# Optimization experiments

Hardware: AMD Instinct MI355X
Metric: run time of the kernel (lower is better)

## Reference

```python
import jax, jax.numpy as jnp
import numpy as np

T, B, I, H = 512, 64, 512, 512


def setup_inputs() -> dict:
    key = jax.random.key(0)
    ks = jax.random.split(key, 24)
    s = (1.0 / H) ** 0.5  # uniform_(-sqrt(1/hidden), sqrt(1/hidden))
    u = lambda k, shape: jax.random.uniform(k, shape, jnp.float32, -s, s)
    inp = {
        "x": jax.random.normal(ks[0], (T, B, I), jnp.float32),
        "h0": u(ks[1], (B, H)),
        "c0": u(ks[2], (B, H)),
    }
    j = 3
    for g in ("ii", "if", "ig", "io"):
        inp["W_" + g] = u(ks[j], (I, H)); j += 1
        inp["b_" + g] = u(ks[j], (H,)); j += 1
    for g in ("hi", "hf", "hg", "ho"):
        inp["W_" + g] = u(ks[j], (H, H)); j += 1
        inp["b_" + g] = u(ks[j], (H,)); j += 1
    return inp


def reference(x, h0, c0, W_ii, b_ii, W_if, b_if, W_ig, b_ig, W_io, b_io,
              W_hi, b_hi, W_hf, b_hf, W_hg, b_hg, W_ho, b_ho):
    # Concatenating per-gate weights is mathematically identical to the 8
    # separate matmuls + bias adds in the source cell.
    Wx = jnp.concatenate([W_ii, W_if, W_ig, W_io], axis=1)        # [I, 4H]
    Wh = jnp.concatenate([W_hi, W_hf, W_hg, W_ho], axis=1)        # [H, 4H]
    b = jnp.concatenate([b_ii + b_hi, b_if + b_hf, b_ig + b_hg, b_io + b_ho])
    # Precompute all input projections in one big GEMM: [T, B, 4H]
    xg = jnp.einsum('tbi,ih->tbh', x, Wx) + b

    def step(carry, xg_t):
        h, c = carry
        gates = xg_t + h @ Wh                                      # [B, 4H]
        i_g, f_g, g_g, o_g = jnp.split(gates, 4, axis=-1)
        i = jax.nn.sigmoid(i_g)
        f = jax.nn.sigmoid(f_g)
        g = jnp.tanh(g_g)
        o = jax.nn.sigmoid(o_g)
        c1 = f * c + i * g
        h1 = o * c1  # NOTE: source applies o * c_1 WITHOUT tanh(c_1)
        return (h1, c1), h1

    (hT, cT), out = jax.lax.scan(step, (h0, c0), xg)               # out: [T, B, H]
    return (out, hT, cT)
```

## Files before the change

kernel.cpp:

```cpp
#include <hip/hip_runtime.h>
#include <stdint.h>


typedef __attribute__((ext_vector_type(8))) short    short8;
typedef __attribute__((ext_vector_type(4))) float    f32x4;
typedef __attribute__((ext_vector_type(4))) unsigned u32x4;
typedef __attribute__((ext_vector_type(2))) unsigned u32x2;

#define XG_OFF    0ull
#define WBT_OFF   134217728ull
#define BIAS_OFF  136314880ull
#define HW_OFF    136323072ull

static __device__ __forceinline__ unsigned short f2bf(float f) {
  unsigned u = __float_as_uint(f);
  unsigned r = (u + 0x7FFFu + ((u >> 16) & 1u)) >> 16;
  return (unsigned short)r;
}
static __device__ __forceinline__ float bf2f(unsigned short u) {
  return __uint_as_float(((unsigned)u) << 16);
}
static __device__ __forceinline__ float sigmoidf_(float x) {
  return 1.0f / (1.0f + __expf(-x));
}
static __device__ __forceinline__ float tanhf_(float x) {
  return 1.0f - 2.0f / (__expf(2.0f * x) + 1.0f);
}

__global__ void lstm_prep(const float* __restrict__ W_ii, const float* __restrict__ W_if,
                          const float* __restrict__ W_ig, const float* __restrict__ W_io,
                          const float* __restrict__ b_ii, const float* __restrict__ b_if,
                          const float* __restrict__ b_ig, const float* __restrict__ b_io,
                          const float* __restrict__ b_hi, const float* __restrict__ b_hf,
                          const float* __restrict__ b_hg, const float* __restrict__ b_ho,
                          const float* __restrict__ h0, unsigned char* ws)
{
  unsigned short*     WbT  = (unsigned short*)(ws + WBT_OFF);
  float*              bias = (float*)(ws + BIAS_OFF);
  unsigned long long* hw64 = (unsigned long long*)(ws + HW_OFF);

  const int gid = blockIdx.x * blockDim.x + threadIdx.x;
  const int gsz = gridDim.x * blockDim.x;

  for (int i = gid; i < 4 * 512 * 512; i += gsz) {
    int g = i >> 18, rem = i & 262143, c = rem >> 9, k = rem & 511;
    const float* W = (g == 0) ? W_ii : (g == 1) ? W_if : (g == 2) ? W_ig : W_io;
    WbT[(size_t)(g * 512 + c) * 512 + k] = f2bf(W[(size_t)k * 512 + c]);
  }
  for (int i = gid; i < 2048; i += gsz) {
    int g = i >> 9, c = i & 511;
    const float* bi = (g == 0) ? b_ii : (g == 1) ? b_if : (g == 2) ? b_ig : b_io;
    const float* bh = (g == 0) ? b_hi : (g == 1) ? b_hf : (g == 2) ? b_hg : b_ho;
    bias[i] = bi[c] + bh[c];
  }
  for (int i = gid; i < 64 * 256; i += gsz) {
    int r = i >> 8, wc = i & 255;
    int gb = r >> 4, row = r & 15, wsl = wc >> 6, c = wc & 63;
    unsigned lo = f2bf(h0[(size_t)r * 512 + wc * 2]);
    unsigned hi = f2bf(h0[(size_t)r * 512 + wc * 2 + 1]);
    hw64[((size_t)(gb * 4 + wsl) * 16 + row) * 64 + c] =
        (unsigned long long)(lo | (hi << 16));
  }
  for (int i = gid; i < 64 * 256; i += gsz)
    hw64[16384 + i] = 0xFFFFFFFF00000000ull;
}

__global__ __launch_bounds__(256) void xproj_gemm(const float* __restrict__ x,
                                                  unsigned char* ws)
{
  const unsigned short* WbT  = (const unsigned short*)(ws + WBT_OFF);
  const float*          bias = (const float*)(ws + BIAS_OFF);
  unsigned short*       xg   = (unsigned short*)(ws + XG_OFF);

  __shared__ unsigned short As[128 * 64];
  __shared__ unsigned short Bs[128 * 64];

  const int bid  = (int)blockIdx.x;
  const int bidx = (bid & 7) * 512 + (bid >> 3);
  const int bm = bidx >> 4, bn = bidx & 15;
  const int row0 = bm * 128, col0 = bn * 128;

  const int tid = threadIdx.x, lane = tid & 63, w = tid >> 6;
  const int wr = w >> 1, wc = w & 1;

  f32x4 acc[4][4] = {};

  for (int k0 = 0; k0 < 512; k0 += 64) {
    __syncthreads();
#pragma unroll
    for (int u = 0; u < 8; ++u) {
      int idx = u * 256 + tid;
      int r = idx >> 4, quad = idx & 15;
      const float4 v = *reinterpret_cast<const float4*>(
          &x[(size_t)(row0 + r) * 512 + k0 + quad * 4]);
      uint2 p;
      p.x = (unsigned)f2bf(v.x) | ((unsigned)f2bf(v.y) << 16);
      p.y = (unsigned)f2bf(v.z) | ((unsigned)f2bf(v.w) << 16);
      *reinterpret_cast<uint2*>(&As[r * 64 + quad * 4]) = p;
    }
#pragma unroll
    for (int u = 0; u < 4; ++u) {
      int idx = u * 256 + tid;
      int cl = idx >> 3, ch = idx & 7;
      *reinterpret_cast<uint4*>(&Bs[cl * 64 + ch * 8]) =
          *reinterpret_cast<const uint4*>(&WbT[(size_t)(col0 + cl) * 512 + k0 + ch * 8]);
    }
    __syncthreads();
#pragma unroll
    for (int kk = 0; kk < 64; kk += 32) {
      short8 a[4], b[4];
#pragma unroll
      for (int m = 0; m < 4; ++m)
        a[m] = *reinterpret_cast<const short8*>(
            &As[(wr * 64 + m * 16 + (lane & 15)) * 64 + kk + (lane >> 4) * 8]);
#pragma unroll
      for (int n = 0; n < 4; ++n)
        b[n] = *reinterpret_cast<const short8*>(
            &Bs[(wc * 64 + n * 16 + (lane & 15)) * 64 + kk + (lane >> 4) * 8]);
#pragma unroll
      for (int m = 0; m < 4; ++m)
#pragma unroll
        for (int n = 0; n < 4; ++n)
          acc[m][n] = __builtin_amdgcn_mfma_f32_16x16x32_bf16(a[m], b[n], acc[m][n], 0, 0, 0);
    }
  }
#pragma unroll
  for (int m = 0; m < 4; ++m) {
    int rowtile = bm * 8 + wr * 4 + m;
#pragma unroll
    for (int n = 0; n < 4; ++n) {
      int coltile = bn * 8 + wc * 4 + n;
      float bv = bias[coltile * 16 + (lane & 15)];
      uint2 p;
      p.x = (unsigned)f2bf(acc[m][n][0] + bv) | ((unsigned)f2bf(acc[m][n][1] + bv) << 16);
      p.y = (unsigned)f2bf(acc[m][n][2] + bv) | ((unsigned)f2bf(acc[m][n][3] + bv) << 16);
      *reinterpret_cast<uint2*>(&xg[((size_t)rowtile * 128 + coltile) * 256 + lane * 4]) = p;
    }
  }
}

__global__ __launch_bounds__(256, 1) void lstm_rec(
    const float* __restrict__ Whi, const float* __restrict__ Whf,
    const float* __restrict__ Whg, const float* __restrict__ Who,
    const float* __restrict__ c0, unsigned char* ws, float* __restrict__ out)
{
  const int gb = (int)blockIdx.x & 3;
  const int gc = (int)blockIdx.x >> 2;
  const int tid = threadIdx.x, lane = tid & 63, w = tid >> 6;

  const unsigned short* xg = (const unsigned short*)(ws + XG_OFF);
  unsigned long long*   hw64 = (unsigned long long*)(ws + HW_OFF);

  __shared__ unsigned hdat[4][1024];
  __shared__ float glds[2][4][4][16][16];

  short8 bhi[4][4], blo[4][4];
  {
    const int colg = gc * 16 + (lane & 15);
    const int krow = (lane >> 4) * 8;
#pragma unroll
    for (int g = 0; g < 4; ++g) {
      const float* P = (g == 0) ? Whi : (g == 1) ? Whf : (g == 2) ? Whg : Who;
#pragma unroll
      for (int kkl = 0; kkl < 4; ++kkl) {
        short8 h8, l8;
#pragma unroll
        for (int i = 0; i < 8; ++i) {
          int k = w * 128 + kkl * 32 + krow + i;
          float wv = P[(size_t)k * 512 + colg];
          unsigned short hb = f2bf(wv);
          h8[i] = (short)hb;
          l8[i] = (short)f2bf(wv - bf2f(hb));
        }
        bhi[g][kkl] = h8; blo[g][kkl] = l8;
      }
    }
  }

  const int crow = tid >> 4, ccol = tid & 15;
  float c = c0[(size_t)(gb * 16 + crow) * 512 + gc * 16 + ccol];

  float* hT = out + 16777216;
  float* cT = out + 16777216 + 32768;
  const int e_ix = (crow >> 2) * 64 + ccol * 4 + (crow & 3);
  int bleft = 30000000;

  for (int t = 0; t < 512; ++t) {
    const size_t xb = (size_t)(t * 4 + gb) * 128 * 256;
    float xgi = bf2f(xg[xb + (size_t)(0 * 32 + gc) * 256 + e_ix]);
    float xgf = bf2f(xg[xb + (size_t)(1 * 32 + gc) * 256 + e_ix]);
    float xgg = bf2f(xg[xb + (size_t)(2 * 32 + gc) * 256 + e_ix]);
    float xgo = bf2f(xg[xb + (size_t)(3 * 32 + gc) * 256 + e_ix]);

    const int par = t & 1;
    const unsigned long long* blk =
        hw64 + (size_t)((par * 4 + gb) * 4 + w) * 1024;
    const unsigned tagw = (unsigned)t;

    u32x4 dv[8];
    const char* lbase = (const char*)blk + lane * 16;
    for (;;) {
#pragma unroll
      for (int i = 0; i < 8; ++i)
        asm volatile("global_load_dwordx4 %0, %1, off sc0 sc1"
                     : "=v"(dv[i]) : "v"(lbase + (size_t)i * 1024));
      asm volatile("s_waitcnt vmcnt(0)"
                   : "+v"(dv[0]), "+v"(dv[1]), "+v"(dv[2]), "+v"(dv[3]),
                     "+v"(dv[4]), "+v"(dv[5]), "+v"(dv[6]), "+v"(dv[7])
                   :: "memory");
      bool ok = true;
#pragma unroll
      for (int i = 0; i < 8; ++i)
        ok = ok && (dv[i][1] == tagw) && (dv[i][3] == tagw);
      if (__all(ok) || --bleft <= 0) break;
      __builtin_amdgcn_s_sleep(1);
    }

#pragma unroll
    for (int i = 0; i < 8; ++i) {
      int k = i * 128 + lane * 2;
      int row = k >> 6;
      int sw = k ^ ((row & 7) << 2);
      u32x2 p2; p2[0] = dv[i][0]; p2[1] = dv[i][2];
      *reinterpret_cast<u32x2*>(&hdat[w][sw]) = p2;
    }
    asm volatile("s_waitcnt lgkmcnt(0)" ::: "memory");
    __builtin_amdgcn_sched_barrier(0);

    f32x4 acc[4] = {};
#pragma unroll
    for (int kkl = 0; kkl < 4; ++kkl) {
      int base = (lane & 15) * 64 + kkl * 16 + (lane >> 4) * 4;
      int sw = base ^ ((lane & 7) << 2);
      union { u32x4 v; short8 s; } fr;
      fr.v = *reinterpret_cast<const u32x4*>(&hdat[w][sw]);
#pragma unroll
      for (int g = 0; g < 4; ++g) {
        acc[g] = __builtin_amdgcn_mfma_f32_16x16x32_bf16(fr.s, bhi[g][kkl], acc[g], 0, 0, 0);
        acc[g] = __builtin_amdgcn_mfma_f32_16x16x32_bf16(fr.s, blo[g][kkl], acc[g], 0, 0, 0);
      }
    }
#pragma unroll
    for (int g = 0; g < 4; ++g)
#pragma unroll
      for (int j = 0; j < 4; ++j)
        glds[par][w][g][(lane >> 4) * 4 + j][lane & 15] = acc[g][j];
    __syncthreads();

    float gi = xgi, gf = xgf, gg = xgg, go = xgo;
#pragma unroll
    for (int ww = 0; ww < 4; ++ww) {
      gi += glds[par][ww][0][crow][ccol];
      gf += glds[par][ww][1][crow][ccol];
      gg += glds[par][ww][2][crow][ccol];
      go += glds[par][ww][3][crow][ccol];
    }
    float iv = sigmoidf_(gi), fv = sigmoidf_(gf), gv = tanhf_(gg), ov = sigmoidf_(go);
    c = fv * c + iv * gv;
    float h = ov * c;

    if (t != 511) {
      float hp = __shfl_xor(h, 1);
      if ((ccol & 1) == 0) {
        unsigned data = (unsigned)f2bf(h) | ((unsigned)f2bf(hp) << 16);
        u32x2 wp; wp[0] = data; wp[1] = (unsigned)(t + 1);
        unsigned long long* dst =
            hw64 + ((size_t)((((t + 1) & 1) * 4 + gb) * 4 + (gc >> 3)) * 16 + crow) * 64 +
            (gc & 7) * 8 + (ccol >> 1);
        asm volatile("global_store_dwordx2 %0, %1, off sc0 sc1"
                     :: "v"(dst), "v"(wp) : "memory");
      }
    }

    out[(size_t)t * 32768 + (size_t)(gb * 16 + crow) * 512 + gc * 16 + ccol] = h;
    if (t == 511) {
      hT[(size_t)(gb * 16 + crow) * 512 + gc * 16 + ccol] = h;
      cT[(size_t)(gb * 16 + crow) * 512 + gc * 16 + ccol] = c;
    }
  }
}

extern "C" void kernel_launch(void* const* d_in, const int* in_sizes, int n_in,
                              void* d_out, int out_size, void* d_ws, size_t ws_size,
                              hipStream_t stream)
{
  const float* x    = (const float*)d_in[0];
  const float* h0   = (const float*)d_in[1];
  const float* c0   = (const float*)d_in[2];
  const float* W_ii = (const float*)d_in[3];
  const float* b_ii = (const float*)d_in[4];
  const float* W_if = (const float*)d_in[5];
  const float* b_if = (const float*)d_in[6];
  const float* W_ig = (const float*)d_in[7];
  const float* b_ig = (const float*)d_in[8];
  const float* W_io = (const float*)d_in[9];
  const float* b_io = (const float*)d_in[10];
  const float* W_hi = (const float*)d_in[11];
  const float* b_hi = (const float*)d_in[12];
  const float* W_hf = (const float*)d_in[13];
  const float* b_hf = (const float*)d_in[14];
  const float* W_hg = (const float*)d_in[15];
  const float* b_hg = (const float*)d_in[16];
  const float* W_ho = (const float*)d_in[17];
  const float* b_ho = (const float*)d_in[18];
  unsigned char* ws = (unsigned char*)d_ws;
  float* out = (float*)d_out;

  hipLaunchKernelGGL(lstm_prep, dim3(1024), dim3(256), 0, stream,
                     W_ii, W_if, W_ig, W_io, b_ii, b_if, b_ig, b_io,
                     b_hi, b_hf, b_hg, b_ho, h0, ws);
  hipLaunchKernelGGL(xproj_gemm, dim3(4096), dim3(256), 0, stream, x, ws);
  hipLaunchKernelGGL(lstm_rec, dim3(128), dim3(256), 0, stream,
                     W_hi, W_hf, W_hg, W_ho, c0, ws, out);
}
```

Baseline: 1.103 ms.

## Tile weight transpose through LDS, drop spin sleep, widen h stores

```diff
diff --git a/kernel.cpp b/kernel.cpp
--- a/kernel.cpp
+++ b/kernel.cpp
@@ -27,42 +27,67 @@
   return 1.0f - 2.0f / (__expf(2.0f * x) + 1.0f);
 }
 
-__global__ void lstm_prep(const float* __restrict__ W_ii, const float* __restrict__ W_if,
-                          const float* __restrict__ W_ig, const float* __restrict__ W_io,
-                          const float* __restrict__ b_ii, const float* __restrict__ b_if,
-                          const float* __restrict__ b_ig, const float* __restrict__ b_io,
-                          const float* __restrict__ b_hi, const float* __restrict__ b_hf,
-                          const float* __restrict__ b_hg, const float* __restrict__ b_ho,
-                          const float* __restrict__ h0, unsigned char* ws)
+__global__ __launch_bounds__(256) void lstm_prep(
+    const float* __restrict__ W_ii, const float* __restrict__ W_if,
+    const float* __restrict__ W_ig, const float* __restrict__ W_io,
+    const float* __restrict__ b_ii, const float* __restrict__ b_if,
+    const float* __restrict__ b_ig, const float* __restrict__ b_io,
+    const float* __restrict__ b_hi, const float* __restrict__ b_hf,
+    const float* __restrict__ b_hg, const float* __restrict__ b_ho,
+    const float* __restrict__ h0, unsigned char* ws)
 {
   unsigned short*     WbT  = (unsigned short*)(ws + WBT_OFF);
   float*              bias = (float*)(ws + BIAS_OFF);
   unsigned long long* hw64 = (unsigned long long*)(ws + HW_OFF);
 
-  const int gid = blockIdx.x * blockDim.x + threadIdx.x;
-  const int gsz = gridDim.x * blockDim.x;
-
-  for (int i = gid; i < 4 * 512 * 512; i += gsz) {
-    int g = i >> 18, rem = i & 262143, c = rem >> 9, k = rem & 511;
-    const float* W = (g == 0) ? W_ii : (g == 1) ? W_if : (g == 2) ? W_ig : W_io;
-    WbT[(size_t)(g * 512 + c) * 512 + k] = f2bf(W[(size_t)k * 512 + c]);
-  }
-  for (int i = gid; i < 2048; i += gsz) {
-    int g = i >> 9, c = i & 511;
-    const float* bi = (g == 0) ? b_ii : (g == 1) ? b_if : (g == 2) ? b_ig : b_io;
-    const float* bh = (g == 0) ? b_hi : (g == 1) ? b_hf : (g == 2) ? b_hg : b_ho;
+  const int bid = (int)blockIdx.x, tid = threadIdx.x;
+
+  __shared__ float lds[32][33];
+
+  const int g  = bid >> 8;
+  const int tr = (bid >> 4) & 15;
+  const int tc = bid & 15;
+  const float* W = (g == 0) ? W_ii : (g == 1) ? W_if : (g == 2) ? W_ig : W_io;
+
+  {
+    const int kl = tid >> 3;
+    const int c4 = (tid & 7) * 4;
+    const float4 v = *reinterpret_cast<const float4*>(
+        &W[(size_t)(tr * 32 + kl) * 512 + tc * 32 + c4]);
+    lds[c4 + 0][kl] = v.x;
+    lds[c4 + 1][kl] = v.y;
+    lds[c4 + 2][kl] = v.z;
+    lds[c4 + 3][kl] = v.w;
+  }
+  __syncthreads();
+  {
+    const int cl = tid >> 3;
+    const int k4 = (tid & 7) * 4;
+    const int gcol = g * 512 + tc * 32 + cl;
+    uint2 p;
+    p.x = (unsigned)f2bf(lds[cl][k4 + 0]) | ((unsigned)f2bf(lds[cl][k4 + 1]) << 16);
+    p.y = (unsigned)f2bf(lds[cl][k4 + 2]) | ((unsigned)f2bf(lds[cl][k4 + 3]) << 16);
+    *reinterpret_cast<uint2*>(&WbT[(size_t)gcol * 512 + tr * 32 + k4]) = p;
+  }
+
+  if (bid < 8) {
+    int i = bid * 256 + tid;
+    int gg = i >> 9, c = i & 511;
+    const float* bi = (gg == 0) ? b_ii : (gg == 1) ? b_if : (gg == 2) ? b_ig : b_io;
+    const float* bh = (gg == 0) ? b_hi : (gg == 1) ? b_hf : (gg == 2) ? b_hg : b_ho;
     bias[i] = bi[c] + bh[c];
-  }
-  for (int i = gid; i < 64 * 256; i += gsz) {
+  } else if (bid >= 64 && bid < 128) {
+    int i = (bid - 64) * 256 + tid;
     int r = i >> 8, wc = i & 255;
     int gb = r >> 4, row = r & 15, wsl = wc >> 6, c = wc & 63;
     unsigned lo = f2bf(h0[(size_t)r * 512 + wc * 2]);
     unsigned hi = f2bf(h0[(size_t)r * 512 + wc * 2 + 1]);
     hw64[((size_t)(gb * 4 + wsl) * 16 + row) * 64 + c] =
         (unsigned long long)(lo | (hi << 16));
-  }
-  for (int i = gid; i < 64 * 256; i += gsz)
+  } else if (bid >= 128 && bid < 192) {
+    int i = (bid - 128) * 256 + tid;
     hw64[16384 + i] = 0xFFFFFFFF00000000ull;
+  }
 }
 
 __global__ __launch_bounds__(256) void xproj_gemm(const float* __restrict__ x,
@@ -213,7 +238,6 @@
       for (int i = 0; i < 8; ++i)
         ok = ok && (dv[i][1] == tagw) && (dv[i][3] == tagw);
       if (__all(ok) || --bleft <= 0) break;
-      __builtin_amdgcn_s_sleep(1);
     }
 
 #pragma unroll
@@ -260,14 +284,17 @@
     float h = ov * c;
 
     if (t != 511) {
-      float hp = __shfl_xor(h, 1);
-      if ((ccol & 1) == 0) {
-        unsigned data = (unsigned)f2bf(h) | ((unsigned)f2bf(hp) << 16);
-        u32x2 wp; wp[0] = data; wp[1] = (unsigned)(t + 1);
+      float h1 = __shfl_xor(h, 1);
+      unsigned pack01 = (unsigned)f2bf(h) | ((unsigned)f2bf(h1) << 16);
+      unsigned pack23 = (unsigned)__shfl_xor((int)pack01, 2);
+      if ((ccol & 3) == 0) {
+        u32x4 wp;
+        wp[0] = pack01; wp[1] = (unsigned)(t + 1);
+        wp[2] = pack23; wp[3] = (unsigned)(t + 1);
         unsigned long long* dst =
             hw64 + ((size_t)((((t + 1) & 1) * 4 + gb) * 4 + (gc >> 3)) * 16 + crow) * 64 +
             (gc & 7) * 8 + (ccol >> 1);
-        asm volatile("global_store_dwordx2 %0, %1, off sc0 sc1"
+        asm volatile("global_store_dwordx4 %0, %1, off sc0 sc1"
                      :: "v"(dst), "v"(wp) : "memory");
       }
     }
```

Result: no change. 1.118 ms (+1.4%).
